# Performance work log

Hardware: AMD Instinct MI355X
Metric: run time of the kernel (lower is better)

The kernel has to match this reference:

```python
import jax, jax.numpy as jnp
import numpy as np
from math import sqrt, pi


def _coeffs(period):
    # Faithful to the torch code, including cos(sqrt(2)*180/period) (radians).
    a1 = jnp.exp(-sqrt(2.0) * pi / period)
    c3 = -a1 ** 2
    c2 = -2.0 * a1 * jnp.cos(sqrt(2.0) * 180.0 / period)
    c1 = (1.0 + c2 - c3) / 4.0
    return c1, c2, c3


def setup_inputs() -> dict:
    key = jax.random.key(0)
    X = jax.random.normal(key, (32, 8192, 256), dtype=jnp.float32)  # (B, T, D)
    period = jnp.array(20.0, dtype=jnp.float32)
    return {"X": X, "period": period}


def reference(X, period):
    c1, c2, c3 = _coeffs(period)
    Xt = jnp.transpose(X, (1, 0, 2))  # (T, B, D)
    T = Xt.shape[0]
    # Per-step inputs for t = 3 .. T-1: X[t-1], X[t-2], X[t-3]
    xs = (Xt[2:T - 1], Xt[1:T - 2], Xt[0:T - 3])

    def step(carry, xin):
        s1, s2 = carry  # X_smooth[t-1], X_smooth[t-2]
        xp1, xp2, xp3 = xin
        s = ((1.0 - c1) * xp1 + (2.0 * c1 - c2) * xp2 - (c1 + c3) * xp3
             + c2 * s1 + c3 * s2)
        return (s, s1), s

    # First 3 timesteps of X_smooth are just X (the clone is never overwritten there).
    _, ys = jax.lax.scan(step, (Xt[2], Xt[1]), xs)
    out = jnp.concatenate([Xt[:3], ys], axis=0)  # (T, B, D)
    return jnp.transpose(out, (1, 0, 2))  # (B, T, D)
```

## Files before the change

### kernel.cpp

```cpp
#include <hip/hip_runtime.h>
#include <math.h>


typedef float f4 __attribute__((ext_vector_type(4)));

#define TT 8192
#define BB 32
#define DD 256
#define LCH 256
#define WARM 48
#define NCH (TT / LCH)
#define ROW (DD / 4)

__device__ __forceinline__ f4 iir4(const f4& xm1, const f4& xm2, const f4& xm3,
                                   const f4& s1, const f4& s2,
                                   float b1, float b2, float b3, float c2, float c3) {
    f4 r;
#pragma unroll
    for (int c = 0; c < 4; ++c) {
        float tmp = fmaf(b3, xm3[c], fmaf(b2, xm2[c], b1 * xm1[c]));
        r[c] = fmaf(c3, s2[c], fmaf(c2, s1[c], tmp));
    }
    return r;
}

template <bool STORE>
__device__ __forceinline__ void run_span(const f4* __restrict__ xp, f4* __restrict__ op,
                                         int ta, int tb,
                                         f4& xm1, f4& xm2, f4& xm3, f4& s1, f4& s2,
                                         float b1, float b2, float b3, float c2, float c3) {
    f4 cur[8], nxt[8];
#pragma unroll
    for (int i = 0; i < 8; ++i) cur[i] = xp[(size_t)(ta + i) * ROW];
    for (int t = ta; t < tb; t += 8) {
        const bool pf = (t + 8) < tb;
        if (pf) {
#pragma unroll
            for (int i = 0; i < 8; ++i) nxt[i] = xp[(size_t)(t + 8 + i) * ROW];
        }
#pragma unroll
        for (int i = 0; i < 8; ++i) {
            f4 s = iir4(xm1, xm2, xm3, s1, s2, b1, b2, b3, c2, c3);
            if (STORE) __builtin_nontemporal_store(s, &op[(size_t)(t + i) * ROW]);
            s2 = s1; s1 = s;
            xm3 = xm2; xm2 = xm1; xm1 = cur[i];
        }
        if (pf) {
#pragma unroll
            for (int i = 0; i < 8; ++i) cur[i] = nxt[i];
        }
    }
}

__global__ __launch_bounds__(64) void ultsmooth_kernel(const f4* __restrict__ X,
                                                       const float* __restrict__ periodp,
                                                       f4* __restrict__ out) {
    const int task  = blockIdx.x;
    const int b     = task / NCH;
    const int chunk = task % NCH;
    const int lane  = threadIdx.x;

    const double p   = (double)periodp[0];
    const double a1  = exp(-1.4142135623730951 * M_PI / p);
    const double dc2 = -2.0 * a1 * cos(1.4142135623730951 * 180.0 / p);
    const double dc3 = -a1 * a1;
    const double dc1 = (1.0 + dc2 - dc3) * 0.25;
    const float b1 = (float)(1.0 - dc1);
    const float b2 = (float)(2.0 * dc1 - dc2);
    const float b3 = (float)(-(dc1 + dc3));
    const float c2 = (float)dc2;
    const float c3 = (float)dc3;

    const f4* xp = X   + (size_t)b * TT * ROW + lane;
    f4*       op = out + (size_t)b * TT * ROW + lane;

    f4 xm1, xm2, xm3, s1, s2;
    const int t0 = chunk * LCH;

    if (chunk == 0) {
        f4 x[8];
#pragma unroll
        for (int i = 0; i < 8; ++i) x[i] = xp[(size_t)i * ROW];
        __builtin_nontemporal_store(x[0], &op[0]);
        __builtin_nontemporal_store(x[1], &op[ROW]);
        __builtin_nontemporal_store(x[2], &op[2 * ROW]);
        xm1 = x[2]; xm2 = x[1]; xm3 = x[0];
        s1 = x[2];  s2 = x[1];
#pragma unroll
        for (int t = 3; t < 8; ++t) {
            f4 s = iir4(xm1, xm2, xm3, s1, s2, b1, b2, b3, c2, c3);
            __builtin_nontemporal_store(s, &op[(size_t)t * ROW]);
            s2 = s1; s1 = s;
            xm3 = xm2; xm2 = xm1; xm1 = x[t];
        }
        run_span<true>(xp, op, 8, LCH, xm1, xm2, xm3, s1, s2, b1, b2, b3, c2, c3);
    } else {
        const int tw = t0 - WARM;
        xm1 = xp[(size_t)(tw - 1) * ROW];
        xm2 = xp[(size_t)(tw - 2) * ROW];
        xm3 = xp[(size_t)(tw - 3) * ROW];
        s1 = xm1; s2 = xm2;
        run_span<false>(xp, op, tw, t0, xm1, xm2, xm3, s1, s2, b1, b2, b3, c2, c3);
        run_span<true>(xp, op, t0, t0 + LCH, xm1, xm2, xm3, s1, s2, b1, b2, b3, c2, c3);
    }
}

extern "C" void kernel_launch(void* const* d_in, const int* in_sizes, int n_in,
                              void* d_out, int out_size, void* d_ws, size_t ws_size,
                              hipStream_t stream) {
    const f4*    X      = (const f4*)d_in[0];
    const float* period = (const float*)d_in[1];
    f4*          out    = (f4*)d_out;

    dim3 grid(BB * NCH);
    dim3 block(64);
    hipLaunchKernelGGL(ultsmooth_kernel, grid, block, 0, stream, X, period, out);
}
```

Before: 91.07 us.

## Triple-buffer input loads, merge warmup and store spans, double chunk length

Replaces the double-buffered load loop with a three-buffer rotation that prefetches two 8-step blocks ahead, so more loads are in flight for the latency-bound recurrence. The warmup span and the stored span are merged into one loop with a runtime store threshold. The chunk length doubles to 512, which halves the grid and the redundant warmup work per output but leaves fewer blocks to hide memory latency. More live registers may lower occupancy.

```diff
diff --git a/kernel.cpp b/kernel.cpp
--- a/kernel.cpp
+++ b/kernel.cpp
@@ -7,7 +7,7 @@
 #define TT 8192
 #define BB 32
 #define DD 256
-#define LCH 256
+#define LCH 512
 #define WARM 48
 #define NCH (TT / LCH)
 #define ROW (DD / 4)
@@ -24,31 +24,52 @@
     return r;
 }
 
-template <bool STORE>
+#define LOADB(BUF, bk)                                                         \
+    do {                                                                       \
+        if ((bk) < nb) {                                                       \
+            _Pragma("unroll") for (int i = 0; i < 8; ++i)                      \
+                BUF[i] = xp[(size_t)(ta + (bk) * 8 + i) * ROW];                \
+        }                                                                      \
+    } while (0)
+
+#define STEPB(BUF)                                                             \
+    do {                                                                       \
+        const int bt = ta + k * 8;                                             \
+        if (bt >= store_from) {                                                \
+            _Pragma("unroll") for (int i = 0; i < 8; ++i) {                    \
+                f4 s = iir4(xm1, xm2, xm3, s1, s2, b1, b2, b3, c2, c3);        \
+                __builtin_nontemporal_store(s, &op[(size_t)(bt + i) * ROW]);   \
+                s2 = s1; s1 = s;                                               \
+                xm3 = xm2; xm2 = xm1; xm1 = BUF[i];                            \
+            }                                                                  \
+        } else {                                                               \
+            _Pragma("unroll") for (int i = 0; i < 8; ++i) {                    \
+                f4 s = iir4(xm1, xm2, xm3, s1, s2, b1, b2, b3, c2, c3);        \
+                s2 = s1; s1 = s;                                               \
+                xm3 = xm2; xm2 = xm1; xm1 = BUF[i];                            \
+            }                                                                  \
+        }                                                                      \
+        ++k;                                                                   \
+    } while (0)
+
 __device__ __forceinline__ void run_span(const f4* __restrict__ xp, f4* __restrict__ op,
-                                         int ta, int tb,
+                                         int ta, int tb, int store_from,
                                          f4& xm1, f4& xm2, f4& xm3, f4& s1, f4& s2,
                                          float b1, float b2, float b3, float c2, float c3) {
-    f4 cur[8], nxt[8];
-#pragma unroll
-    for (int i = 0; i < 8; ++i) cur[i] = xp[(size_t)(ta + i) * ROW];
-    for (int t = ta; t < tb; t += 8) {
-        const bool pf = (t + 8) < tb;
-        if (pf) {
-#pragma unroll
-            for (int i = 0; i < 8; ++i) nxt[i] = xp[(size_t)(t + 8 + i) * ROW];
-        }
-#pragma unroll
-        for (int i = 0; i < 8; ++i) {
-            f4 s = iir4(xm1, xm2, xm3, s1, s2, b1, b2, b3, c2, c3);
-            if (STORE) __builtin_nontemporal_store(s, &op[(size_t)(t + i) * ROW]);
-            s2 = s1; s1 = s;
-            xm3 = xm2; xm2 = xm1; xm1 = cur[i];
-        }
-        if (pf) {
-#pragma unroll
-            for (int i = 0; i < 8; ++i) cur[i] = nxt[i];
-        }
+    const int nb = (tb - ta) / 8;
+    f4 bA[8], bB[8], bC[8];
+    LOADB(bA, 0);
+    LOADB(bB, 1);
+    int k = 0;
+    while (k < nb) {
+        LOADB(bC, k + 2);
+        STEPB(bA);
+        if (k >= nb) break;
+        LOADB(bA, k + 2);
+        STEPB(bB);
+        if (k >= nb) break;
+        LOADB(bB, k + 2);
+        STEPB(bC);
     }
 }
 
@@ -93,15 +114,14 @@
             s2 = s1; s1 = s;
             xm3 = xm2; xm2 = xm1; xm1 = x[t];
         }
-        run_span<true>(xp, op, 8, LCH, xm1, xm2, xm3, s1, s2, b1, b2, b3, c2, c3);
+        run_span(xp, op, 8, LCH, 0, xm1, xm2, xm3, s1, s2, b1, b2, b3, c2, c3);
     } else {
         const int tw = t0 - WARM;
         xm1 = xp[(size_t)(tw - 1) * ROW];
         xm2 = xp[(size_t)(tw - 2) * ROW];
         xm3 = xp[(size_t)(tw - 3) * ROW];
         s1 = xm1; s2 = xm2;
-        run_span<false>(xp, op, tw, t0, xm1, xm2, xm3, s1, s2, b1, b2, b3, c2, c3);
-        run_span<true>(xp, op, t0, t0 + LCH, xm1, xm2, xm3, s1, s2, b1, b2, b3, c2, c3);
+        run_span(xp, op, tw, t0 + LCH, t0, xm1, xm2, xm3, s1, s2, b1, b2, b3, c2, c3);
     }
 }
 
```

Result: faster. 87.63 us (-3.8%).
